# Performance work log

Hardware: AMD Instinct MI355X
Metric: run time of the kernel (lower is better)

## Reference

```python
import jax, jax.numpy as jnp
import numpy as np

D_MODEL = 1024
N_HEADS = 16
HEAD_DIM = D_MODEL // N_HEADS


def setup_inputs() -> dict:
    key = jax.random.key(0)
    ks = jax.random.split(key, 12)
    B, S = 2, 2048
    scale = 1.0 / np.sqrt(D_MODEL)
    inp = {
        "query": jax.random.normal(ks[0], (B, S, D_MODEL), jnp.float32),
        "key": jax.random.normal(ks[1], (B, S, D_MODEL), jnp.float32),
        "value": jax.random.normal(ks[2], (B, S, D_MODEL), jnp.float32),
        "Wq": jax.random.normal(ks[3], (D_MODEL, D_MODEL), jnp.float32) * scale,
        "bq": jnp.zeros((D_MODEL,), jnp.float32),
        "Wk": jax.random.normal(ks[4], (D_MODEL, D_MODEL), jnp.float32) * scale,
        "bk": jnp.zeros((D_MODEL,), jnp.float32),
        "Wv": jax.random.normal(ks[5], (D_MODEL, D_MODEL), jnp.float32) * scale,
        "bv": jnp.zeros((D_MODEL,), jnp.float32),
        "Wo": jax.random.normal(ks[6], (D_MODEL, D_MODEL), jnp.float32) * scale,
        "bo": jnp.zeros((D_MODEL,), jnp.float32),
    }
    return inp


def _split_heads(x):
    # [B, S, D] -> [B, H, S, Dh]
    B, S, _ = x.shape
    return x.reshape(B, S, N_HEADS, HEAD_DIM).transpose(0, 2, 1, 3)


def reference(query, key, value, Wq, bq, Wk, bk, Wv, bv, Wo, bo):
    B, S, _ = query.shape
    Q = _split_heads(query @ Wq + bq)   # [B,H,S,Dh]
    K = _split_heads(key @ Wk + bk)
    V = _split_heads(value @ Wv + bv)
    inv_sqrt_dh = 1.0 / np.sqrt(HEAD_DIM).astype(np.float32)
    scores = jnp.einsum("bhqd,bhkd->bhqk", Q, K) * inv_sqrt_dh
    attention = jax.nn.softmax(scores, axis=-1)
    # dropout is identity in eval mode
    out = jnp.einsum("bhqk,bhkd->bhqd", attention, V)
    out = out.transpose(0, 2, 1, 3).reshape(B, S, D_MODEL)
    out = out @ Wo + bo
    return out, attention
```

## Files before the change

kernel.cpp:

```cpp
#include <hip/hip_runtime.h>
#include <math.h>

#define D_MODEL 1024
#define NHEADS 16
#define HDIM 64
#define BATCH 2
#define SEQ 2048
#define MROWS (BATCH * SEQ)

typedef unsigned int uint32;
typedef __attribute__((ext_vector_type(8))) short short8;
typedef __attribute__((ext_vector_type(4))) float f32x4;
typedef __attribute__((ext_vector_type(16))) float f32x16;
typedef __attribute__((ext_vector_type(2))) unsigned int uint2v;

__device__ __forceinline__ unsigned short f2bf(float f) {
  unsigned int u = __float_as_uint(f);
  u += 0x7fffu + ((u >> 16) & 1u);
  return (unsigned short)(u >> 16);
}

__device__ __forceinline__ float fexp2(float x) {
  float r;
  asm("v_exp_f32 %0, %1" : "=v"(r) : "v"(x));
  return r;
}

__device__ __forceinline__ unsigned int cvtpk(float lo, float hi) {
  unsigned int r;
  asm("v_cvt_pk_bf16_f32 %0, %1, %2" : "=v"(r) : "v"(lo), "v"(hi));
  return r;
}

__device__ __forceinline__ void bar_lgkm() {
  asm volatile("s_waitcnt lgkmcnt(0)\n\ts_barrier" ::: "memory");
}

__device__ __forceinline__ void gl_lds16(const void* g, void* l) {
  __builtin_amdgcn_global_load_lds((const __attribute__((address_space(1))) void*)g,
                                   (__attribute__((address_space(3))) void*)l, 16, 0, 0);
}

__global__ __launch_bounds__(256) void conv_kernel(const float* q, const float* k, const float* v,
                                                   unsigned short* xq, unsigned short* xk,
                                                   unsigned short* xv) {
  int z = blockIdx.y;
  const float* s = (z == 0) ? q : ((z == 1) ? k : v);
  unsigned short* d = (z == 0) ? xq : ((z == 1) ? xk : xv);
  int i = (blockIdx.x * 256 + threadIdx.x) * 8;
  float4 v0 = *(const float4*)(s + i);
  float4 v1 = *(const float4*)(s + i + 4);
  uint4 o;
  o.x = cvtpk(v0.x, v0.y);
  o.y = cvtpk(v0.z, v0.w);
  o.z = cvtpk(v1.x, v1.y);
  o.w = cvtpk(v1.z, v1.w);
  *(uint4*)(d + i) = o;
}

struct WtArgs { const float* src[4]; };

__global__ __launch_bounds__(256) void wt_kernel(WtArgs args, unsigned short* dst) {
  const float* W = args.src[blockIdx.z];
  unsigned short* WT = dst + (size_t)blockIdx.z * (D_MODEL * D_MODEL);
  __shared__ unsigned short tile[64][80];
  int t = threadIdx.x;
  int r = t >> 2, cc = (t & 3) * 16;
  int k0 = blockIdx.y * 64, n0 = blockIdx.x * 64;
  const float* src = W + (size_t)(k0 + r) * D_MODEL + n0 + cc;
#pragma unroll
  for (int j = 0; j < 16; j += 4) {
    float4 v = *(const float4*)(src + j);
    tile[r][cc + j + 0] = f2bf(v.x);
    tile[r][cc + j + 1] = f2bf(v.y);
    tile[r][cc + j + 2] = f2bf(v.z);
    tile[r][cc + j + 3] = f2bf(v.w);
  }
  __syncthreads();
  __align__(16) unsigned short tmp[16];
#pragma unroll
  for (int j = 0; j < 16; ++j) tmp[j] = tile[cc + j][r];
  unsigned short* d = WT + (size_t)(n0 + r) * D_MODEL + k0 + cc;
  *(uint4*)d = ((uint4*)tmp)[0];
  *(uint4*)(d + 8) = ((uint4*)tmp)[1];
}

struct GemmArgs {
  const unsigned short* A[3];
  const unsigned short* W[3];
  const float* bias[3];
  void* C[3];
};

template <bool OUT_F32>
__global__ __launch_bounds__(256) void gemm_kernel(GemmArgs args) {
  int bid = blockIdx.x;
  int wgid = (bid & 7) * (gridDim.x >> 3) + (bid >> 3);
  int x = wgid & 7;
  int yz = wgid >> 3;
  int y = yz & 31;
  int z = yz >> 5;
  const unsigned short* A = args.A[z];
  const unsigned short* WT = args.W[z];
  const float* bias = args.bias[z];
  int n0 = x * 128, m0 = y * 128;
  __shared__ __align__(16) unsigned short As[128 * 64];
  __shared__ __align__(16) unsigned short Bs[128 * 64];
  int t = threadIdx.x;
  int wave = t >> 6, lane = t & 63;
  int wm = (wave >> 1) * 64, wn = (wave & 1) * 64;
  int lr = lane & 15, lg = lane >> 4;
  int r8 = lane >> 3, c8 = (lane & 7) * 8;
  f32x4 acc[4][4] = {};

  for (int kt = 0; kt < D_MODEL; kt += 64) {
#pragma unroll
    for (int i = 0; i < 4; ++i) {
      int row = wave * 32 + i * 8;
      gl_lds16(A + (size_t)(m0 + row + r8) * D_MODEL + kt + c8, As + row * 64);
      gl_lds16(WT + (size_t)(n0 + row + r8) * D_MODEL + kt + c8, Bs + row * 64);
    }
    __syncthreads();
    short8 af[4][2], bf[4][2];
#pragma unroll
    for (int f = 0; f < 4; ++f) {
#pragma unroll
      for (int kk = 0; kk < 2; ++kk) {
        af[f][kk] = *(const short8*)((const char*)As + (wm + f * 16 + lr) * 128 + kk * 64 + lg * 16);
        bf[f][kk] = *(const short8*)((const char*)Bs + (wn + f * 16 + lr) * 128 + kk * 64 + lg * 16);
      }
    }
#pragma unroll
    for (int i = 0; i < 4; ++i)
#pragma unroll
      for (int j = 0; j < 4; ++j)
#pragma unroll
        for (int kk = 0; kk < 2; ++kk)
          acc[i][j] = __builtin_amdgcn_mfma_f32_16x16x32_bf16(af[i][kk], bf[j][kk], acc[i][j], 0, 0, 0);
    __syncthreads();
  }
#pragma unroll
  for (int i = 0; i < 4; ++i)
#pragma unroll
    for (int j = 0; j < 4; ++j) {
      int col = n0 + wn + j * 16 + lr;
      float bb = bias[col];
#pragma unroll
      for (int r = 0; r < 4; ++r) {
        int row = m0 + wm + i * 16 + lg * 4 + r;
        float v = acc[i][j][r] + bb;
        if (OUT_F32)
          ((float*)args.C[z])[(size_t)row * D_MODEL + col] = v;
        else
          ((unsigned short*)args.C[z])[(size_t)row * D_MODEL + col] = f2bf(v);
      }
    }
}

__global__ __launch_bounds__(256) void vt_kernel(const unsigned short* V, unsigned short* Vt) {
  int bh = blockIdx.y;
  int b = bh >> 4;
  int h = bh & 15;
  int s0 = blockIdx.x * 64;
  __shared__ unsigned short tile[64][80];
  int t = threadIdx.x;
  int r = t >> 2, c = (t & 3) * 16;
  const unsigned short* src = V + (size_t)(b * SEQ + s0 + r) * D_MODEL + h * HDIM + c;
  __align__(16) unsigned short buf[16];
  ((uint4*)buf)[0] = *(const uint4*)src;
  ((uint4*)buf)[1] = *(const uint4*)(src + 8);
#pragma unroll
  for (int j = 0; j < 16; ++j) tile[r][c + j] = buf[j];
  __syncthreads();
  __align__(16) unsigned short tmp[16];
#pragma unroll
  for (int j = 0; j < 16; ++j) tmp[j] = tile[c + j][r];
  unsigned short* dst = Vt + ((size_t)bh * HDIM + r) * SEQ + s0 + c;
  *(uint4*)dst = ((uint4*)tmp)[0];
  *(uint4*)(dst + 8) = ((uint4*)tmp)[1];
}

__global__ __launch_bounds__(256) void attn_kernel(const unsigned short* Q, const unsigned short* K,
                                                   const unsigned short* Vt, float* attn,
                                                   unsigned short* ctx) {
  int bid = blockIdx.x;
  int wgid = (bid & 7) * 64 + (bid >> 3);
  int bh = wgid >> 4;
  int q0 = (wgid & 15) * 128;
  int b = bh >> 4, h = bh & 15;
  int t = threadIdx.x, wave = t >> 6, lane = t & 63;
  int l31 = lane & 31, hi = lane >> 5;

  __shared__ __align__(16) char Ks[2][64 * 128];
  __shared__ __align__(16) char Vs[2][64 * 128];

  const unsigned short* Kp = K + (size_t)(b * SEQ) * D_MODEL + h * HDIM;
  const unsigned short* Vp = Vt + (size_t)bh * HDIM * SEQ;

  short8 qv[4];
  {
    const unsigned short* qp = Q + (size_t)(b * SEQ + q0 + wave * 32 + l31) * D_MODEL + h * HDIM + hi * 8;
#pragma unroll
    for (int kk = 0; kk < 4; ++kk) qv[kk] = *(const short8*)(qp + kk * 16);
  }

  const float SCL = 0.125f * 1.44269504f;
  float lsum = 0.f;
  f32x16 oacc[2] = {};

#pragma unroll
  for (int c = 0; c < 2; ++c) {
    int idx = t + 256 * c;
    int row = idx >> 3, ch = idx & 7;
    int cb = (ch * 16) ^ ((row & 7) << 4);
    *(uint4*)(Ks[0] + row * 128 + cb) = *(const uint4*)(Kp + (size_t)row * D_MODEL + ch * 8);
    *(uint4*)(Vs[0] + row * 128 + cb) = *(const uint4*)(Vp + (size_t)row * SEQ + ch * 8);
  }
  bar_lgkm();
  int cur = 0;
  for (int ti = 0; ti < 32; ++ti) {
    uint4 nk[2], nv[2];
    bool more = (ti + 1) < 32;
    if (more) {
#pragma unroll
      for (int c = 0; c < 2; ++c) {
        int idx = t + 256 * c;
        int row = idx >> 3, ch = idx & 7;
        nk[c] = *(const uint4*)(Kp + (size_t)((ti + 1) * 64 + row) * D_MODEL + ch * 8);
        nv[c] = *(const uint4*)(Vp + (size_t)row * SEQ + (ti + 1) * 64 + ch * 8);
      }
    }
    f32x16 st[2] = {};
#pragma unroll
    for (int n = 0; n < 2; ++n)
#pragma unroll
      for (int kk = 0; kk < 4; ++kk) {
        int kr = n * 32 + l31;
        short8 ak = *(const short8*)(Ks[cur] + kr * 128 + ((kk * 32 + hi * 16) ^ ((kr & 7) << 4)));
        st[n] = __builtin_amdgcn_mfma_f32_32x32x16_bf16(ak, qv[kk], st[n], 0, 0, 0);
      }
    unsigned int P0[2][4], P1[2][4];
#pragma unroll
    for (int n = 0; n < 2; ++n)
#pragma unroll
      for (int j2 = 0; j2 < 4; ++j2) {
        float p0 = fexp2(st[n][4 * j2 + 0] * SCL);
        float p1 = fexp2(st[n][4 * j2 + 1] * SCL);
        float p2 = fexp2(st[n][4 * j2 + 2] * SCL);
        float p3 = fexp2(st[n][4 * j2 + 3] * SCL);
        lsum += (p0 + p1) + (p2 + p3);
        P0[n][j2] = cvtpk(p0, p1);
        P1[n][j2] = cvtpk(p2, p3);
      }
    short8 pa[4];
#pragma unroll
    for (int n = 0; n < 2; ++n)
#pragma unroll
      for (int c = 0; c < 2; ++c) {
        uint2v s0 = __builtin_amdgcn_permlane32_swap(P0[n][2 * c], P0[n][2 * c + 1], false, false);
        uint2v s1 = __builtin_amdgcn_permlane32_swap(P1[n][2 * c], P1[n][2 * c + 1], false, false);
        uint4 w;
        w.x = s0.x; w.y = s1.x; w.z = s0.y; w.w = s1.y;
        pa[n * 2 + c] = *(short8*)&w;
      }
#pragma unroll
    for (int n2 = 0; n2 < 2; ++n2)
#pragma unroll
      for (int kk = 0; kk < 4; ++kk) {
        int vr = n2 * 32 + l31;
        short8 bv = *(const short8*)(Vs[cur] + vr * 128 + ((kk * 32 + hi * 16) ^ ((vr & 7) << 4)));
        oacc[n2] = __builtin_amdgcn_mfma_f32_32x32x16_bf16(pa[kk], bv, oacc[n2], 0, 0, 0);
      }
    if (more) {
#pragma unroll
      for (int c = 0; c < 2; ++c) {
        int idx = t + 256 * c;
        int row = idx >> 3, ch = idx & 7;
        int cb = (ch * 16) ^ ((row & 7) << 4);
        *(uint4*)(Ks[cur ^ 1] + row * 128 + cb) = nk[c];
        *(uint4*)(Vs[cur ^ 1] + row * 128 + cb) = nv[c];
      }
    }
    bar_lgkm();
    cur ^= 1;
  }
  float tot = lsum + __shfl_xor(lsum, 32, 64);
  float inv = 1.f / tot;
  float iv16[16];
#pragma unroll
  for (int reg = 0; reg < 16; ++reg) {
    int qr = (reg & 3) + 8 * (reg >> 2) + 4 * hi;
    iv16[reg] = __shfl(inv, qr, 64);
  }
#pragma unroll
  for (int n2 = 0; n2 < 2; ++n2)
#pragma unroll
    for (int reg = 0; reg < 16; ++reg) {
      int qr = (reg & 3) + 8 * (reg >> 2) + 4 * hi;
      int row = b * SEQ + q0 + wave * 32 + qr;
      ctx[(size_t)row * D_MODEL + h * HDIM + n2 * 32 + l31] = f2bf(oacc[n2][reg] * iv16[reg]);
    }

  float* rowp[16];
  {
    float* abase = attn + (size_t)bh * SEQ * SEQ + l31;
#pragma unroll
    for (int reg = 0; reg < 16; ++reg) {
      int qr = (reg & 3) + 8 * (reg >> 2) + 4 * hi;
      rowp[reg] = abase + (size_t)(q0 + wave * 32 + qr) * SEQ;
    }
  }
#pragma unroll
  for (int c = 0; c < 2; ++c) {
    int idx = t + 256 * c;
    int row = idx >> 3, ch = idx & 7;
    int cb = (ch * 16) ^ ((row & 7) << 4);
    *(uint4*)(Ks[0] + row * 128 + cb) = *(const uint4*)(Kp + (size_t)row * D_MODEL + ch * 8);
  }
  bar_lgkm();
  cur = 0;
  for (int ti = 0; ti < 32; ++ti) {
    uint4 nk[2];
    bool more = (ti + 1) < 32;
    if (more) {
#pragma unroll
      for (int c = 0; c < 2; ++c) {
        int idx = t + 256 * c;
        int row = idx >> 3, ch = idx & 7;
        nk[c] = *(const uint4*)(Kp + (size_t)((ti + 1) * 64 + row) * D_MODEL + ch * 8);
      }
    }
    f32x16 st[2] = {};
#pragma unroll
    for (int n = 0; n < 2; ++n)
#pragma unroll
      for (int kk = 0; kk < 4; ++kk) {
        int kr = n * 32 + l31;
        short8 bk = *(const short8*)(Ks[cur] + kr * 128 + ((kk * 32 + hi * 16) ^ ((kr & 7) << 4)));
        st[n] = __builtin_amdgcn_mfma_f32_32x32x16_bf16(qv[kk], bk, st[n], 0, 0, 0);
      }
#pragma unroll
    for (int n = 0; n < 2; ++n)
#pragma unroll
      for (int reg = 0; reg < 16; ++reg) {
        float p = fexp2(st[n][reg] * SCL) * iv16[reg];
        __builtin_nontemporal_store(p, rowp[reg] + ti * 64 + n * 32);
      }
    if (more) {
#pragma unroll
      for (int c = 0; c < 2; ++c) {
        int idx = t + 256 * c;
        int row = idx >> 3, ch = idx & 7;
        int cb = (ch * 16) ^ ((row & 7) << 4);
        *(uint4*)(Ks[cur ^ 1] + row * 128 + cb) = nk[c];
      }
    }
    bar_lgkm();
    cur ^= 1;
  }
}

extern "C" void kernel_launch(void* const* d_in, const int* in_sizes, int n_in,
                              void* d_out, int out_size, void* d_ws, size_t ws_size,
                              hipStream_t stream) {
  const float* query = (const float*)d_in[0];
  const float* key   = (const float*)d_in[1];
  const float* value = (const float*)d_in[2];
  const float* Wq = (const float*)d_in[3];
  const float* bq = (const float*)d_in[4];
  const float* Wk = (const float*)d_in[5];
  const float* bk = (const float*)d_in[6];
  const float* Wv = (const float*)d_in[7];
  const float* bv = (const float*)d_in[8];
  const float* Wo = (const float*)d_in[9];
  const float* bo = (const float*)d_in[10];

  char* ws = (char*)d_ws;
  const size_t MB = (size_t)1 << 20;
  unsigned short* WqT = (unsigned short*)(ws + 0 * MB);
  unsigned short* WkT = (unsigned short*)(ws + 2 * MB);
  unsigned short* WvT = (unsigned short*)(ws + 4 * MB);
  unsigned short* WoT = (unsigned short*)(ws + 6 * MB);
  unsigned short* Xq  = (unsigned short*)(ws + 8 * MB);
  unsigned short* Xk  = (unsigned short*)(ws + 16 * MB);
  unsigned short* Xv  = (unsigned short*)(ws + 24 * MB);
  unsigned short* Qw  = (unsigned short*)(ws + 32 * MB);
  unsigned short* Kw  = (unsigned short*)(ws + 40 * MB);
  unsigned short* Vw  = (unsigned short*)(ws + 48 * MB);
  unsigned short* Vtw = (unsigned short*)(ws + 16 * MB);
  unsigned short* Cw  = (unsigned short*)(ws + 8 * MB);

  float* out0 = (float*)d_out;
  float* attn = out0 + (size_t)MROWS * D_MODEL;

  conv_kernel<<<dim3(2048, 3), 256, 0, stream>>>(query, key, value, Xq, Xk, Xv);

  WtArgs wa;
  wa.src[0] = Wq; wa.src[1] = Wk; wa.src[2] = Wv; wa.src[3] = Wo;
  wt_kernel<<<dim3(16, 16, 4), 256, 0, stream>>>(wa, WqT);

  GemmArgs ga;
  ga.A[0] = Xq; ga.A[1] = Xk; ga.A[2] = Xv;
  ga.W[0] = WqT; ga.W[1] = WkT; ga.W[2] = WvT;
  ga.bias[0] = bq; ga.bias[1] = bk; ga.bias[2] = bv;
  ga.C[0] = Qw; ga.C[1] = Kw; ga.C[2] = Vw;
  gemm_kernel<false><<<dim3(768), 256, 0, stream>>>(ga);

  vt_kernel<<<dim3(32, 32), 256, 0, stream>>>(Vw, Vtw);

  attn_kernel<<<dim3(512), 256, 0, stream>>>(Qw, Kw, Vtw, attn, Cw);

  GemmArgs go;
  go.A[0] = Cw; go.A[1] = Cw; go.A[2] = Cw;
  go.W[0] = WoT; go.W[1] = WoT; go.W[2] = WoT;
  go.bias[0] = bo; go.bias[1] = bo; go.bias[2] = bo;
  go.C[0] = d_out; go.C[1] = d_out; go.C[2] = d_out;
  gemm_kernel<true><<<dim3(256), 256, 0, stream>>>(go);
}
```

Baseline: 285.6 us.

## Split attention into context and weights kernels, read K/V directly from global

Result: slower. 354.4 us (+24.1%).

```diff
diff --git a/kernel.cpp b/kernel.cpp
--- a/kernel.cpp
+++ b/kernel.cpp
@@ -30,10 +30,6 @@
   unsigned int r;
   asm("v_cvt_pk_bf16_f32 %0, %1, %2" : "=v"(r) : "v"(lo), "v"(hi));
   return r;
-}
-
-__device__ __forceinline__ void bar_lgkm() {
-  asm volatile("s_waitcnt lgkmcnt(0)\n\ts_barrier" ::: "memory");
 }
 
 __device__ __forceinline__ void gl_lds16(const void* g, void* l) {
@@ -180,9 +176,9 @@
   *(uint4*)(dst + 8) = ((uint4*)tmp)[1];
 }
 
-__global__ __launch_bounds__(256) void attn_kernel(const unsigned short* Q, const unsigned short* K,
-                                                   const unsigned short* Vt, float* attn,
-                                                   unsigned short* ctx) {
+__global__ __launch_bounds__(256, 3) void attn_ctx_kernel(const unsigned short* Q, const unsigned short* K,
+                                                          const unsigned short* Vt, float* invl_g,
+                                                          unsigned short* ctx) {
   int bid = blockIdx.x;
   int wgid = (bid & 7) * 64 + (bid >> 3);
   int bh = wgid >> 4;
@@ -191,11 +187,8 @@
   int t = threadIdx.x, wave = t >> 6, lane = t & 63;
   int l31 = lane & 31, hi = lane >> 5;
 
-  __shared__ __align__(16) char Ks[2][64 * 128];
-  __shared__ __align__(16) char Vs[2][64 * 128];
-
-  const unsigned short* Kp = K + (size_t)(b * SEQ) * D_MODEL + h * HDIM;
-  const unsigned short* Vp = Vt + (size_t)bh * HDIM * SEQ;
+  const unsigned short* Kf = K + (size_t)(b * SEQ + l31) * D_MODEL + h * HDIM + hi * 8;
+  const unsigned short* Vf = Vt + ((size_t)bh * HDIM + l31) * SEQ + hi * 8;
 
   short8 qv[4];
   {
@@ -208,35 +201,13 @@
   float lsum = 0.f;
   f32x16 oacc[2] = {};
 
-#pragma unroll
-  for (int c = 0; c < 2; ++c) {
-    int idx = t + 256 * c;
-    int row = idx >> 3, ch = idx & 7;
-    int cb = (ch * 16) ^ ((row & 7) << 4);
-    *(uint4*)(Ks[0] + row * 128 + cb) = *(const uint4*)(Kp + (size_t)row * D_MODEL + ch * 8);
-    *(uint4*)(Vs[0] + row * 128 + cb) = *(const uint4*)(Vp + (size_t)row * SEQ + ch * 8);
-  }
-  bar_lgkm();
-  int cur = 0;
   for (int ti = 0; ti < 32; ++ti) {
-    uint4 nk[2], nv[2];
-    bool more = (ti + 1) < 32;
-    if (more) {
-#pragma unroll
-      for (int c = 0; c < 2; ++c) {
-        int idx = t + 256 * c;
-        int row = idx >> 3, ch = idx & 7;
-        nk[c] = *(const uint4*)(Kp + (size_t)((ti + 1) * 64 + row) * D_MODEL + ch * 8);
-        nv[c] = *(const uint4*)(Vp + (size_t)row * SEQ + (ti + 1) * 64 + ch * 8);
-      }
-    }
     f32x16 st[2] = {};
 #pragma unroll
     for (int n = 0; n < 2; ++n)
 #pragma unroll
       for (int kk = 0; kk < 4; ++kk) {
-        int kr = n * 32 + l31;
-        short8 ak = *(const short8*)(Ks[cur] + kr * 128 + ((kk * 32 + hi * 16) ^ ((kr & 7) << 4)));
+        short8 ak = *(const short8*)(Kf + (size_t)(ti * 64 + n * 32) * D_MODEL + kk * 16);
         st[n] = __builtin_amdgcn_mfma_f32_32x32x16_bf16(ak, qv[kk], st[n], 0, 0, 0);
       }
     unsigned int P0[2][4], P1[2][4];
@@ -267,25 +238,13 @@
     for (int n2 = 0; n2 < 2; ++n2)
 #pragma unroll
       for (int kk = 0; kk < 4; ++kk) {
-        int vr = n2 * 32 + l31;
-        short8 bv = *(const short8*)(Vs[cur] + vr * 128 + ((kk * 32 + hi * 16) ^ ((vr & 7) << 4)));
+        short8 bv = *(const short8*)(Vf + (size_t)(n2 * 32) * SEQ + ti * 64 + kk * 16);
         oacc[n2] = __builtin_amdgcn_mfma_f32_32x32x16_bf16(pa[kk], bv, oacc[n2], 0, 0, 0);
       }
-    if (more) {
-#pragma unroll
-      for (int c = 0; c < 2; ++c) {
-        int idx = t + 256 * c;
-        int row = idx >> 3, ch = idx & 7;
-        int cb = (ch * 16) ^ ((row & 7) << 4);
-        *(uint4*)(Ks[cur ^ 1] + row * 128 + cb) = nk[c];
-        *(uint4*)(Vs[cur ^ 1] + row * 128 + cb) = nv[c];
-      }
-    }
-    bar_lgkm();
-    cur ^= 1;
   }
   float tot = lsum + __shfl_xor(lsum, 32, 64);
   float inv = 1.f / tot;
+  if (lane < 32) invl_g[(size_t)bh * SEQ + q0 + wave * 32 + l31] = inv;
   float iv16[16];
 #pragma unroll
   for (int reg = 0; reg < 16; ++reg) {
@@ -300,63 +259,51 @@
       int row = b * SEQ + q0 + wave * 32 + qr;
       ctx[(size_t)row * D_MODEL + h * HDIM + n2 * 32 + l31] = f2bf(oacc[n2][reg] * iv16[reg]);
     }
-
-  float* rowp[16];
+}
+
+__global__ __launch_bounds__(256, 4) void attn_w_kernel(const unsigned short* Q, const unsigned short* K,
+                                                        const float* invl_g, float* attn) {
+  int bid = blockIdx.x;
+  int wgid = (bid & 7) * 64 + (bid >> 3);
+  int bh = wgid >> 4;
+  int q0 = (wgid & 15) * 128;
+  int b = bh >> 4, h = bh & 15;
+  int t = threadIdx.x, wave = t >> 6, lane = t & 63;
+  int l31 = lane & 31, hi = lane >> 5;
+
+  const unsigned short* Kf = K + (size_t)(b * SEQ + l31) * D_MODEL + h * HDIM + hi * 8;
+
+  short8 qv[4];
   {
-    float* abase = attn + (size_t)bh * SEQ * SEQ + l31;
-#pragma unroll
-    for (int reg = 0; reg < 16; ++reg) {
-      int qr = (reg & 3) + 8 * (reg >> 2) + 4 * hi;
-      rowp[reg] = abase + (size_t)(q0 + wave * 32 + qr) * SEQ;
-    }
-  }
-#pragma unroll
-  for (int c = 0; c < 2; ++c) {
-    int idx = t + 256 * c;
-    int row = idx >> 3, ch = idx & 7;
-    int cb = (ch * 16) ^ ((row & 7) << 4);
-    *(uint4*)(Ks[0] + row * 128 + cb) = *(const uint4*)(Kp + (size_t)row * D_MODEL + ch * 8);
-  }
-  bar_lgkm();
-  cur = 0;
+    const unsigned short* qp = Q + (size_t)(b * SEQ + q0 + wave * 32 + l31) * D_MODEL + h * HDIM + hi * 8;
+#pragma unroll
+    for (int kk = 0; kk < 4; ++kk) qv[kk] = *(const short8*)(qp + kk * 16);
+  }
+  float4 invl4[4];
+#pragma unroll
+  for (int j2 = 0; j2 < 4; ++j2)
+    invl4[j2] = *(const float4*)(invl_g + (size_t)bh * SEQ + q0 + wave * 32 + 8 * j2 + 4 * hi);
+
+  float* abase = attn + (size_t)bh * SEQ * SEQ + (size_t)(q0 + wave * 32 + 4 * hi) * SEQ + l31;
+  const float SCL = 0.125f * 1.44269504f;
+
   for (int ti = 0; ti < 32; ++ti) {
-    uint4 nk[2];
-    bool more = (ti + 1) < 32;
-    if (more) {
-#pragma unroll
-      for (int c = 0; c < 2; ++c) {
-        int idx = t + 256 * c;
-        int row = idx >> 3, ch = idx & 7;
-        nk[c] = *(const uint4*)(Kp + (size_t)((ti + 1) * 64 + row) * D_MODEL + ch * 8);
-      }
-    }
     f32x16 st[2] = {};
 #pragma unroll
     for (int n = 0; n < 2; ++n)
 #pragma unroll
       for (int kk = 0; kk < 4; ++kk) {
-        int kr = n * 32 + l31;
-        short8 bk = *(const short8*)(Ks[cur] + kr * 128 + ((kk * 32 + hi * 16) ^ ((kr & 7) << 4)));
+        short8 bk = *(const short8*)(Kf + (size_t)(ti * 64 + n * 32) * D_MODEL + kk * 16);
         st[n] = __builtin_amdgcn_mfma_f32_32x32x16_bf16(qv[kk], bk, st[n], 0, 0, 0);
       }
+    float* tb = abase + ti * 64;
 #pragma unroll
     for (int n = 0; n < 2; ++n)
 #pragma unroll
       for (int reg = 0; reg < 16; ++reg) {
-        float p = fexp2(st[n][reg] * SCL) * iv16[reg];
-        __builtin_nontemporal_store(p, rowp[reg] + ti * 64 + n * 32);
-      }
-    if (more) {
-#pragma unroll
-      for (int c = 0; c < 2; ++c) {
-        int idx = t + 256 * c;
-        int row = idx >> 3, ch = idx & 7;
-        int cb = (ch * 16) ^ ((row & 7) << 4);
-        *(uint4*)(Ks[cur ^ 1] + row * 128 + cb) = nk[c];
-      }
-    }
-    bar_lgkm();
-    cur ^= 1;
+        float p = fexp2(st[n][reg] * SCL) * invl4[reg >> 2][reg & 3];
+        __builtin_nontemporal_store(p, tb + ((reg & 3) + 8 * (reg >> 2)) * SEQ + n * 32);
+      }
   }
 }
 
@@ -389,6 +336,7 @@
   unsigned short* Vw  = (unsigned short*)(ws + 48 * MB);
   unsigned short* Vtw = (unsigned short*)(ws + 16 * MB);
   unsigned short* Cw  = (unsigned short*)(ws + 8 * MB);
+  float* invl_g       = (float*)(ws + 56 * MB);
 
   float* out0 = (float*)d_out;
   float* attn = out0 + (size_t)MROWS * D_MODEL;
@@ -408,7 +356,8 @@
 
   vt_kernel<<<dim3(32, 32), 256, 0, stream>>>(Vw, Vtw);
 
-  attn_kernel<<<dim3(512), 256, 0, stream>>>(Qw, Kw, Vtw, attn, Cw);
+  attn_ctx_kernel<<<dim3(512), 256, 0, stream>>>(Qw, Kw, Vtw, invl_g, Cw);
+  attn_w_kernel<<<dim3(512), 256, 0, stream>>>(Qw, Kw, invl_g, attn);
 
   GemmArgs go;
   go.A[0] = Cw; go.A[1] = Cw; go.A[2] = Cw;
```

## Fuse prep kernels and compute V transposed directly in QKV GEMM

Applied to the files above, without the earlier changes.

After: 280.2 us. No clear change (-1.9%).

```diff
diff --git a/kernel.cpp b/kernel.cpp
--- a/kernel.cpp
+++ b/kernel.cpp
@@ -41,48 +41,54 @@
                                    (__attribute__((address_space(3))) void*)l, 16, 0, 0);
 }
 
-__global__ __launch_bounds__(256) void conv_kernel(const float* q, const float* k, const float* v,
-                                                   unsigned short* xq, unsigned short* xk,
-                                                   unsigned short* xv) {
-  int z = blockIdx.y;
-  const float* s = (z == 0) ? q : ((z == 1) ? k : v);
-  unsigned short* d = (z == 0) ? xq : ((z == 1) ? xk : xv);
-  int i = (blockIdx.x * 256 + threadIdx.x) * 8;
-  float4 v0 = *(const float4*)(s + i);
-  float4 v1 = *(const float4*)(s + i + 4);
-  uint4 o;
-  o.x = cvtpk(v0.x, v0.y);
-  o.y = cvtpk(v0.z, v0.w);
-  o.z = cvtpk(v1.x, v1.y);
-  o.w = cvtpk(v1.z, v1.w);
-  *(uint4*)(d + i) = o;
-}
-
-struct WtArgs { const float* src[4]; };
-
-__global__ __launch_bounds__(256) void wt_kernel(WtArgs args, unsigned short* dst) {
-  const float* W = args.src[blockIdx.z];
-  unsigned short* WT = dst + (size_t)blockIdx.z * (D_MODEL * D_MODEL);
-  __shared__ unsigned short tile[64][80];
+struct PrepArgs {
+  const float* act[3];
+  unsigned short* actout[3];
+  const float* w[4];
+  unsigned short* wout;
+};
+
+__global__ __launch_bounds__(256) void prep_kernel(PrepArgs args) {
+  int bid = blockIdx.x;
   int t = threadIdx.x;
-  int r = t >> 2, cc = (t & 3) * 16;
-  int k0 = blockIdx.y * 64, n0 = blockIdx.x * 64;
-  const float* src = W + (size_t)(k0 + r) * D_MODEL + n0 + cc;
-#pragma unroll
-  for (int j = 0; j < 16; j += 4) {
-    float4 v = *(const float4*)(src + j);
-    tile[r][cc + j + 0] = f2bf(v.x);
-    tile[r][cc + j + 1] = f2bf(v.y);
-    tile[r][cc + j + 2] = f2bf(v.z);
-    tile[r][cc + j + 3] = f2bf(v.w);
-  }
-  __syncthreads();
-  __align__(16) unsigned short tmp[16];
-#pragma unroll
-  for (int j = 0; j < 16; ++j) tmp[j] = tile[cc + j][r];
-  unsigned short* d = WT + (size_t)(n0 + r) * D_MODEL + k0 + cc;
-  *(uint4*)d = ((uint4*)tmp)[0];
-  *(uint4*)(d + 8) = ((uint4*)tmp)[1];
+  if (bid < 6144) {
+    int z = bid >> 11, blk = bid & 2047;
+    const float* s = args.act[z];
+    unsigned short* d = args.actout[z];
+    int i = (blk * 256 + t) * 8;
+    float4 v0 = *(const float4*)(s + i);
+    float4 v1 = *(const float4*)(s + i + 4);
+    uint4 o;
+    o.x = cvtpk(v0.x, v0.y);
+    o.y = cvtpk(v0.z, v0.w);
+    o.z = cvtpk(v1.x, v1.y);
+    o.w = cvtpk(v1.z, v1.w);
+    *(uint4*)(d + i) = o;
+  } else {
+    __shared__ unsigned short tile[64][80];
+    int wb = bid - 6144;
+    int zz = wb >> 8, rem = wb & 255;
+    int n0 = (rem & 15) * 64, k0 = (rem >> 4) * 64;
+    const float* W = args.w[zz];
+    unsigned short* WT = args.wout + (size_t)zz * (D_MODEL * D_MODEL);
+    int r = t >> 2, cc = (t & 3) * 16;
+    const float* src = W + (size_t)(k0 + r) * D_MODEL + n0 + cc;
+#pragma unroll
+    for (int j = 0; j < 16; j += 4) {
+      float4 v = *(const float4*)(src + j);
+      tile[r][cc + j + 0] = f2bf(v.x);
+      tile[r][cc + j + 1] = f2bf(v.y);
+      tile[r][cc + j + 2] = f2bf(v.z);
+      tile[r][cc + j + 3] = f2bf(v.w);
+    }
+    __syncthreads();
+    __align__(16) unsigned short tmp[16];
+#pragma unroll
+    for (int j = 0; j < 16; ++j) tmp[j] = tile[cc + j][r];
+    unsigned short* d = WT + (size_t)(n0 + r) * D_MODEL + k0 + cc;
+    *(uint4*)d = ((uint4*)tmp)[0];
+    *(uint4*)(d + 8) = ((uint4*)tmp)[1];
+  }
 }
 
 struct GemmArgs {
@@ -92,17 +98,273 @@
   void* C[3];
 };
 
-template <bool OUT_F32>
-__global__ __launch_bounds__(256) void gemm_kernel(GemmArgs args) {
+__global__ __launch_bounds__(256) void gemm_qkv_kernel(GemmArgs args) {
   int bid = blockIdx.x;
-  int wgid = (bid & 7) * (gridDim.x >> 3) + (bid >> 3);
-  int x = wgid & 7;
-  int yz = wgid >> 3;
-  int y = yz & 31;
-  int z = yz >> 5;
-  const unsigned short* A = args.A[z];
-  const unsigned short* WT = args.W[z];
-  const float* bias = args.bias[z];
+  int wgid = (bid & 7) * 96 + (bid >> 3);
+  const unsigned short *A, *WT;
+  const float* bias;
+  void* C;
+  int m0, n0;
+  bool vtrans;
+  if (wgid < 512) {
+    int x = wgid & 7, yz = wgid >> 3, y = yz & 31, z = yz >> 5;
+    A = args.A[z]; WT = args.W[z]; bias = args.bias[z]; C = args.C[z];
+    n0 = x * 128; m0 = y * 128; vtrans = false;
+  } else {
+    int w2 = wgid - 512, x2 = w2 & 31, y2 = w2 >> 5;
+    A = args.W[2];
+    WT = args.A[2];
+    bias = args.bias[2]; C = args.C[2];
+    n0 = x2 * 128; m0 = y2 * 128; vtrans = true;
+  }
+  __shared__ __align__(16) unsigned short As[128 * 64];
+  __shared__ __align__(16) unsigned short Bs[128 * 64];
+  int t = threadIdx.x;
+  int wave = t >> 6, lane = t & 63;
+  int wm = (wave >> 1) * 64, wn = (wave & 1) * 64;
+  int lr = lane & 15, lg = lane >> 4;
+  int r8 = lane >> 3, c8 = (lane & 7) * 8;
+  f32x4 acc[4][4] = {};
+
+  for (int kt = 0; kt < D_MODEL; kt += 64) {
+#pragma unroll
+    for (int i = 0; i < 4; ++i) {
+      int row = wave * 32 + i * 8;
+      gl_lds16(A + (size_t)(m0 + row + r8) * D_MODEL + kt + c8, As + row * 64);
+      gl_lds16(WT + (size_t)(n0 + row + r8) * D_MODEL + kt + c8, Bs + row * 64);
+    }
+    __syncthreads();
+    short8 af[4][2], bf[4][2];
+#pragma unroll
+    for (int f = 0; f < 4; ++f) {
+#pragma unroll
+      for (int kk = 0; kk < 2; ++kk) {
+        af[f][kk] = *(const short8*)((const char*)As + (wm + f * 16 + lr) * 128 + kk * 64 + lg * 16);
+        bf[f][kk] = *(const short8*)((const char*)Bs + (wn + f * 16 + lr) * 128 + kk * 64 + lg * 16);
+      }
+    }
+#pragma unroll
+    for (int i = 0; i < 4; ++i)
+#pragma unroll
+      for (int j = 0; j < 4; ++j)
+#pragma unroll
+        for (int kk = 0; kk < 2; ++kk)
+          acc[i][j] = __builtin_amdgcn_mfma_f32_16x16x32_bf16(af[i][kk], bf[j][kk], acc[i][j], 0, 0, 0);
+    __syncthreads();
+  }
+  if (!vtrans) {
+#pragma unroll
+    for (int i = 0; i < 4; ++i)
+#pragma unroll
+      for (int j = 0; j < 4; ++j) {
+        int col = n0 + wn + j * 16 + lr;
+        float bb = bias[col];
+#pragma unroll
+        for (int r = 0; r < 4; ++r) {
+          int row = m0 + wm + i * 16 + lg * 4 + r;
+          ((unsigned short*)C)[(size_t)row * D_MODEL + col] = f2bf(acc[i][j][r] + bb);
+        }
+      }
+  } else {
+#pragma unroll
+    for (int i = 0; i < 4; ++i)
+#pragma unroll
+      for (int j = 0; j < 4; ++j) {
+        int col = n0 + wn + j * 16 + lr;
+#pragma unroll
+        for (int r = 0; r < 4; ++r) {
+          int row = m0 + wm + i * 16 + lg * 4 + r;
+          ((unsigned short*)C)[(size_t)row * MROWS + col] = f2bf(acc[i][j][r] + bias[row]);
+        }
+      }
+  }
+}
+
+__global__ __launch_bounds__(256) void attn_kernel(const unsigned short* Q, const unsigned short* K,
+                                                   const unsigned short* Vt2, float* attn,
+                                                   unsigned short* ctx) {
+  int bid = blockIdx.x;
+  int wgid = (bid & 7) * 64 + (bid >> 3);
+  int bh = wgid >> 4;
+  int q0 = (wgid & 15) * 128;
+  int b = bh >> 4, h = bh & 15;
+  int t = threadIdx.x, wave = t >> 6, lane = t & 63;
+  int l31 = lane & 31, hi = lane >> 5;
+
+  __shared__ __align__(16) char Ks[2][64 * 128];
+  __shared__ __align__(16) char Vs[2][64 * 128];
+
+  const unsigned short* Kp = K + (size_t)(b * SEQ) * D_MODEL + h * HDIM;
+  const unsigned short* Vp = Vt2 + (size_t)(h * HDIM) * MROWS + b * SEQ;
+
+  short8 qv[4];
+  {
+    const unsigned short* qp = Q + (size_t)(b * SEQ + q0 + wave * 32 + l31) * D_MODEL + h * HDIM + hi * 8;
+#pragma unroll
+    for (int kk = 0; kk < 4; ++kk) qv[kk] = *(const short8*)(qp + kk * 16);
+  }
+
+  const float SCL = 0.125f * 1.44269504f;
+  float lsum = 0.f;
+  f32x16 oacc[2] = {};
+
+#pragma unroll
+  for (int c = 0; c < 2; ++c) {
+    int idx = t + 256 * c;
+    int row = idx >> 3, ch = idx & 7;
+    int cb = (ch * 16) ^ ((row & 7) << 4);
+    *(uint4*)(Ks[0] + row * 128 + cb) = *(const uint4*)(Kp + (size_t)row * D_MODEL + ch * 8);
+    *(uint4*)(Vs[0] + row * 128 + cb) = *(const uint4*)(Vp + (size_t)row * MROWS + ch * 8);
+  }
+  bar_lgkm();
+  int cur = 0;
+  for (int ti = 0; ti < 32; ++ti) {
+    uint4 nk[2], nv[2];
+    bool more = (ti + 1) < 32;
+    if (more) {
+#pragma unroll
+      for (int c = 0; c < 2; ++c) {
+        int idx = t + 256 * c;
+        int row = idx >> 3, ch = idx & 7;
+        nk[c] = *(const uint4*)(Kp + (size_t)((ti + 1) * 64 + row) * D_MODEL + ch * 8);
+        nv[c] = *(const uint4*)(Vp + (size_t)row * MROWS + (ti + 1) * 64 + ch * 8);
+      }
+    }
+    f32x16 st[2] = {};
+#pragma unroll
+    for (int n = 0; n < 2; ++n)
+#pragma unroll
+      for (int kk = 0; kk < 4; ++kk) {
+        int kr = n * 32 + l31;
+        short8 ak = *(const short8*)(Ks[cur] + kr * 128 + ((kk * 32 + hi * 16) ^ ((kr & 7) << 4)));
+        st[n] = __builtin_amdgcn_mfma_f32_32x32x16_bf16(ak, qv[kk], st[n], 0, 0, 0);
+      }
+    unsigned int P0[2][4], P1[2][4];
+#pragma unroll
+    for (int n = 0; n < 2; ++n)
+#pragma unroll
+      for (int j2 = 0; j2 < 4; ++j2) {
+        float p0 = fexp2(st[n][4 * j2 + 0] * SCL);
+        float p1 = fexp2(st[n][4 * j2 + 1] * SCL);
+        float p2 = fexp2(st[n][4 * j2 + 2] * SCL);
+        float p3 = fexp2(st[n][4 * j2 + 3] * SCL);
+        lsum += (p0 + p1) + (p2 + p3);
+        P0[n][j2] = cvtpk(p0, p1);
+        P1[n][j2] = cvtpk(p2, p3);
+      }
+    short8 pa[4];
+#pragma unroll
+    for (int n = 0; n < 2; ++n)
+#pragma unroll
+      for (int c = 0; c < 2; ++c) {
+        uint2v s0 = __builtin_amdgcn_permlane32_swap(P0[n][2 * c], P0[n][2 * c + 1], false, false);
+        uint2v s1 = __builtin_amdgcn_permlane32_swap(P1[n][2 * c], P1[n][2 * c + 1], false, false);
+        uint4 w;
+        w.x = s0.x; w.y = s1.x; w.z = s0.y; w.w = s1.y;
+        pa[n * 2 + c] = *(short8*)&w;
+      }
+#pragma unroll
+    for (int n2 = 0; n2 < 2; ++n2)
+#pragma unroll
+      for (int kk = 0; kk < 4; ++kk) {
+        int vr = n2 * 32 + l31;
+        short8 bv = *(const short8*)(Vs[cur] + vr * 128 + ((kk * 32 + hi * 16) ^ ((vr & 7) << 4)));
+        oacc[n2] = __builtin_amdgcn_mfma_f32_32x32x16_bf16(pa[kk], bv, oacc[n2], 0, 0, 0);
+      }
+    if (more) {
+#pragma unroll
+      for (int c = 0; c < 2; ++c) {
+        int idx = t + 256 * c;
+        int row = idx >> 3, ch = idx & 7;
+        int cb = (ch * 16) ^ ((row & 7) << 4);
+        *(uint4*)(Ks[cur ^ 1] + row * 128 + cb) = nk[c];
+        *(uint4*)(Vs[cur ^ 1] + row * 128 + cb) = nv[c];
+      }
+    }
+    bar_lgkm();
+    cur ^= 1;
+  }
+  float tot = lsum + __shfl_xor(lsum, 32, 64);
+  float inv = 1.f / tot;
+  float iv16[16];
+#pragma unroll
+  for (int reg = 0; reg < 16; ++reg) {
+    int qr = (reg & 3) + 8 * (reg >> 2) + 4 * hi;
+    iv16[reg] = __shfl(inv, qr, 64);
+  }
+#pragma unroll
+  for (int n2 = 0; n2 < 2; ++n2)
+#pragma unroll
+    for (int reg = 0; reg < 16; ++reg) {
+      int qr = (reg & 3) + 8 * (reg >> 2) + 4 * hi;
+      int row = b * SEQ + q0 + wave * 32 + qr;
+      ctx[(size_t)row * D_MODEL + h * HDIM + n2 * 32 + l31] = f2bf(oacc[n2][reg] * iv16[reg]);
+    }
+
+  float* rowp[16];
+  {
+    float* abase = attn + (size_t)bh * SEQ * SEQ + l31;
+#pragma unroll
+    for (int reg = 0; reg < 16; ++reg) {
+      int qr = (reg & 3) + 8 * (reg >> 2) + 4 * hi;
+      rowp[reg] = abase + (size_t)(q0 + wave * 32 + qr) * SEQ;
+    }
+  }
+#pragma unroll
+  for (int c = 0; c < 2; ++c) {
+    int idx = t + 256 * c;
+    int row = idx >> 3, ch = idx & 7;
+    int cb = (ch * 16) ^ ((row & 7) << 4);
+    *(uint4*)(Ks[0] + row * 128 + cb) = *(const uint4*)(Kp + (size_t)row * D_MODEL + ch * 8);
+  }
+  bar_lgkm();
+  cur = 0;
+  for (int ti = 0; ti < 32; ++ti) {
+    uint4 nk[2];
+    bool more = (ti + 1) < 32;
+    if (more) {
+#pragma unroll
+      for (int c = 0; c < 2; ++c) {
+        int idx = t + 256 * c;
+        int row = idx >> 3, ch = idx & 7;
+        nk[c] = *(const uint4*)(Kp + (size_t)((ti + 1) * 64 + row) * D_MODEL + ch * 8);
+      }
+    }
+    f32x16 st[2] = {};
+#pragma unroll
+    for (int n = 0; n < 2; ++n)
+#pragma unroll
+      for (int kk = 0; kk < 4; ++kk) {
+        int kr = n * 32 + l31;
+        short8 bk = *(const short8*)(Ks[cur] + kr * 128 + ((kk * 32 + hi * 16) ^ ((kr & 7) << 4)));
+        st[n] = __builtin_amdgcn_mfma_f32_32x32x16_bf16(qv[kk], bk, st[n], 0, 0, 0);
+      }
+#pragma unroll
+    for (int n = 0; n < 2; ++n)
+#pragma unroll
+      for (int reg = 0; reg < 16; ++reg) {
+        float p = fexp2(st[n][reg] * SCL) * iv16[reg];
+        __builtin_nontemporal_store(p, rowp[reg] + ti * 64 + n * 32);
+      }
+    if (more) {
+#pragma unroll
+      for (int c = 0; c < 2; ++c) {
+        int idx = t + 256 * c;
+        int row = idx >> 3, ch = idx & 7;
+        int cb = (ch * 16) ^ ((row & 7) << 4);
+        *(uint4*)(Ks[cur ^ 1] + row * 128 + cb) = nk[c];
+      }
+    }
+    bar_lgkm();
+    cur ^= 1;
+  }
+}
+
+__global__ __launch_bounds__(256) void gemm_o_kernel(const unsigned short* A, const unsigned short* WT,
+                                                     const float* bias, float* C) {
+  int bid = blockIdx.x;
+  int wgid = (bid & 7) * 32 + (bid >> 3);
+  int x = wgid & 7, y = wgid >> 3;
   int n0 = x * 128, m0 = y * 128;
   __shared__ __align__(16) unsigned short As[128 * 64];
   __shared__ __align__(16) unsigned short Bs[128 * 64];
@@ -148,216 +410,9 @@
 #pragma unroll
       for (int r = 0; r < 4; ++r) {
         int row = m0 + wm + i * 16 + lg * 4 + r;
-        float v = acc[i][j][r] + bb;
-        if (OUT_F32)
-          ((float*)args.C[z])[(size_t)row * D_MODEL + col] = v;
-        else
-          ((unsigned short*)args.C[z])[(size_t)row * D_MODEL + col] = f2bf(v);
-      }
-    }
-}
-
-__global__ __launch_bounds__(256) void vt_kernel(const unsigned short* V, unsigned short* Vt) {
-  int bh = blockIdx.y;
-  int b = bh >> 4;
-  int h = bh & 15;
-  int s0 = blockIdx.x * 64;
-  __shared__ unsigned short tile[64][80];
-  int t = threadIdx.x;
-  int r = t >> 2, c = (t & 3) * 16;
-  const unsigned short* src = V + (size_t)(b * SEQ + s0 + r) * D_MODEL + h * HDIM + c;
-  __align__(16) unsigned short buf[16];
-  ((uint4*)buf)[0] = *(const uint4*)src;
-  ((uint4*)buf)[1] = *(const uint4*)(src + 8);
-#pragma unroll
-  for (int j = 0; j < 16; ++j) tile[r][c + j] = buf[j];
-  __syncthreads();
-  __align__(16) unsigned short tmp[16];
-#pragma unroll
-  for (int j = 0; j < 16; ++j) tmp[j] = tile[c + j][r];
-  unsigned short* dst = Vt + ((size_t)bh * HDIM + r) * SEQ + s0 + c;
-  *(uint4*)dst = ((uint4*)tmp)[0];
-  *(uint4*)(dst + 8) = ((uint4*)tmp)[1];
-}
-
-__global__ __launch_bounds__(256) void attn_kernel(const unsigned short* Q, const unsigned short* K,
-                                                   const unsigned short* Vt, float* attn,
-                                                   unsigned short* ctx) {
-  int bid = blockIdx.x;
-  int wgid = (bid & 7) * 64 + (bid >> 3);
-  int bh = wgid >> 4;
-  int q0 = (wgid & 15) * 128;
-  int b = bh >> 4, h = bh & 15;
-  int t = threadIdx.x, wave = t >> 6, lane = t & 63;
-  int l31 = lane & 31, hi = lane >> 5;
-
-  __shared__ __align__(16) char Ks[2][64 * 128];
-  __shared__ __align__(16) char Vs[2][64 * 128];
-
-  const unsigned short* Kp = K + (size_t)(b * SEQ) * D_MODEL + h * HDIM;
-  const unsigned short* Vp = Vt + (size_t)bh * HDIM * SEQ;
-
-  short8 qv[4];
-  {
-    const unsigned short* qp = Q + (size_t)(b * SEQ + q0 + wave * 32 + l31) * D_MODEL + h * HDIM + hi * 8;
-#pragma unroll
-    for (int kk = 0; kk < 4; ++kk) qv[kk] = *(const short8*)(qp + kk * 16);
-  }
-
-  const float SCL = 0.125f * 1.44269504f;
-  float lsum = 0.f;
-  f32x16 oacc[2] = {};
-
-#pragma unroll
-  for (int c = 0; c < 2; ++c) {
-    int idx = t + 256 * c;
-    int row = idx >> 3, ch = idx & 7;
-    int cb = (ch * 16) ^ ((row & 7) << 4);
-    *(uint4*)(Ks[0] + row * 128 + cb) = *(const uint4*)(Kp + (size_t)row * D_MODEL + ch * 8);
-    *(uint4*)(Vs[0] + row * 128 + cb) = *(const uint4*)(Vp + (size_t)row * SEQ + ch * 8);
-  }
-  bar_lgkm();
-  int cur = 0;
-  for (int ti = 0; ti < 32; ++ti) {
-    uint4 nk[2], nv[2];
-    bool more = (ti + 1) < 32;
-    if (more) {
-#pragma unroll
-      for (int c = 0; c < 2; ++c) {
-        int idx = t + 256 * c;
-        int row = idx >> 3, ch = idx & 7;
-        nk[c] = *(const uint4*)(Kp + (size_t)((ti + 1) * 64 + row) * D_MODEL + ch * 8);
-        nv[c] = *(const uint4*)(Vp + (size_t)row * SEQ + (ti + 1) * 64 + ch * 8);
-      }
-    }
-    f32x16 st[2] = {};
-#pragma unroll
-    for (int n = 0; n < 2; ++n)
-#pragma unroll
-      for (int kk = 0; kk < 4; ++kk) {
-        int kr = n * 32 + l31;
-        short8 ak = *(const short8*)(Ks[cur] + kr * 128 + ((kk * 32 + hi * 16) ^ ((kr & 7) << 4)));
-        st[n] = __builtin_amdgcn_mfma_f32_32x32x16_bf16(ak, qv[kk], st[n], 0, 0, 0);
-      }
-    unsigned int P0[2][4], P1[2][4];
-#pragma unroll
-    for (int n = 0; n < 2; ++n)
-#pragma unroll
-      for (int j2 = 0; j2 < 4; ++j2) {
-        float p0 = fexp2(st[n][4 * j2 + 0] * SCL);
-        float p1 = fexp2(st[n][4 * j2 + 1] * SCL);
-        float p2 = fexp2(st[n][4 * j2 + 2] * SCL);
-        float p3 = fexp2(st[n][4 * j2 + 3] * SCL);
-        lsum += (p0 + p1) + (p2 + p3);
-        P0[n][j2] = cvtpk(p0, p1);
-        P1[n][j2] = cvtpk(p2, p3);
-      }
-    short8 pa[4];
-#pragma unroll
-    for (int n = 0; n < 2; ++n)
-#pragma unroll
-      for (int c = 0; c < 2; ++c) {
-        uint2v s0 = __builtin_amdgcn_permlane32_swap(P0[n][2 * c], P0[n][2 * c + 1], false, false);
-        uint2v s1 = __builtin_amdgcn_permlane32_swap(P1[n][2 * c], P1[n][2 * c + 1], false, false);
-        uint4 w;
-        w.x = s0.x; w.y = s1.x; w.z = s0.y; w.w = s1.y;
-        pa[n * 2 + c] = *(short8*)&w;
-      }
-#pragma unroll
-    for (int n2 = 0; n2 < 2; ++n2)
-#pragma unroll
-      for (int kk = 0; kk < 4; ++kk) {
-        int vr = n2 * 32 + l31;
-        short8 bv = *(const short8*)(Vs[cur] + vr * 128 + ((kk * 32 + hi * 16) ^ ((vr & 7) << 4)));
-        oacc[n2] = __builtin_amdgcn_mfma_f32_32x32x16_bf16(pa[kk], bv, oacc[n2], 0, 0, 0);
-      }
-    if (more) {
-#pragma unroll
-      for (int c = 0; c < 2; ++c) {
-        int idx = t + 256 * c;
-        int row = idx >> 3, ch = idx & 7;
-        int cb = (ch * 16) ^ ((row & 7) << 4);
-        *(uint4*)(Ks[cur ^ 1] + row * 128 + cb) = nk[c];
-        *(uint4*)(Vs[cur ^ 1] + row * 128 + cb) = nv[c];
-      }
-    }
-    bar_lgkm();
-    cur ^= 1;
-  }
-  float tot = lsum + __shfl_xor(lsum, 32, 64);
-  float inv = 1.f / tot;
-  float iv16[16];
-#pragma unroll
-  for (int reg = 0; reg < 16; ++reg) {
-    int qr = (reg & 3) + 8 * (reg >> 2) + 4 * hi;
-    iv16[reg] = __shfl(inv, qr, 64);
-  }
-#pragma unroll
-  for (int n2 = 0; n2 < 2; ++n2)
-#pragma unroll
-    for (int reg = 0; reg < 16; ++reg) {
-      int qr = (reg & 3) + 8 * (reg >> 2) + 4 * hi;
-      int row = b * SEQ + q0 + wave * 32 + qr;
-      ctx[(size_t)row * D_MODEL + h * HDIM + n2 * 32 + l31] = f2bf(oacc[n2][reg] * iv16[reg]);
-    }
-
-  float* rowp[16];
-  {
-    float* abase = attn + (size_t)bh * SEQ * SEQ + l31;
-#pragma unroll
-    for (int reg = 0; reg < 16; ++reg) {
-      int qr = (reg & 3) + 8 * (reg >> 2) + 4 * hi;
-      rowp[reg] = abase + (size_t)(q0 + wave * 32 + qr) * SEQ;
-    }
-  }
-#pragma unroll
-  for (int c = 0; c < 2; ++c) {
-    int idx = t + 256 * c;
-    int row = idx >> 3, ch = idx & 7;
-    int cb = (ch * 16) ^ ((row & 7) << 4);
-    *(uint4*)(Ks[0] + row * 128 + cb) = *(const uint4*)(Kp + (size_t)row * D_MODEL + ch * 8);
-  }
-  bar_lgkm();
-  cur = 0;
-  for (int ti = 0; ti < 32; ++ti) {
-    uint4 nk[2];
-    bool more = (ti + 1) < 32;
-    if (more) {
-#pragma unroll
-      for (int c = 0; c < 2; ++c) {
-        int idx = t + 256 * c;
-        int row = idx >> 3, ch = idx & 7;
-        nk[c] = *(const uint4*)(Kp + (size_t)((ti + 1) * 64 + row) * D_MODEL + ch * 8);
-      }
-    }
-    f32x16 st[2] = {};
-#pragma unroll
-    for (int n = 0; n < 2; ++n)
-#pragma unroll
-      for (int kk = 0; kk < 4; ++kk) {
-        int kr = n * 32 + l31;
-        short8 bk = *(const short8*)(Ks[cur] + kr * 128 + ((kk * 32 + hi * 16) ^ ((kr & 7) << 4)));
-        st[n] = __builtin_amdgcn_mfma_f32_32x32x16_bf16(qv[kk], bk, st[n], 0, 0, 0);
-      }
-#pragma unroll
-    for (int n = 0; n < 2; ++n)
-#pragma unroll
-      for (int reg = 0; reg < 16; ++reg) {
-        float p = fexp2(st[n][reg] * SCL) * iv16[reg];
-        __builtin_nontemporal_store(p, rowp[reg] + ti * 64 + n * 32);
-      }
-    if (more) {
-#pragma unroll
-      for (int c = 0; c < 2; ++c) {
-        int idx = t + 256 * c;
-        int row = idx >> 3, ch = idx & 7;
-        int cb = (ch * 16) ^ ((row & 7) << 4);
-        *(uint4*)(Ks[cur ^ 1] + row * 128 + cb) = nk[c];
-      }
-    }
-    bar_lgkm();
-    cur ^= 1;
-  }
+        C[(size_t)row * D_MODEL + col] = acc[i][j][r] + bb;
+      }
+    }
 }
 
 extern "C" void kernel_launch(void* const* d_in, const int* in_sizes, int n_in,
@@ -378,7 +433,6 @@
   char* ws = (char*)d_ws;
   const size_t MB = (size_t)1 << 20;
   unsigned short* WqT = (unsigned short*)(ws + 0 * MB);
-  unsigned short* WkT = (unsigned short*)(ws + 2 * MB);
   unsigned short* WvT = (unsigned short*)(ws + 4 * MB);
   unsigned short* WoT = (unsigned short*)(ws + 6 * MB);
   unsigned short* Xq  = (unsigned short*)(ws + 8 * MB);
@@ -386,34 +440,27 @@
   unsigned short* Xv  = (unsigned short*)(ws + 24 * MB);
   unsigned short* Qw  = (unsigned short*)(ws + 32 * MB);
   unsigned short* Kw  = (unsigned short*)(ws + 40 * MB);
-  unsigned short* Vw  = (unsigned short*)(ws + 48 * MB);
-  unsigned short* Vtw = (unsigned short*)(ws + 16 * MB);
+  unsigned short* Vt2 = (unsigned short*)(ws + 48 * MB);
   unsigned short* Cw  = (unsigned short*)(ws + 8 * MB);
 
   float* out0 = (float*)d_out;
   float* attn = out0 + (size_t)MROWS * D_MODEL;
 
-  conv_kernel<<<dim3(2048, 3), 256, 0, stream>>>(query, key, value, Xq, Xk, Xv);
-
-  WtArgs wa;
-  wa.src[0] = Wq; wa.src[1] = Wk; wa.src[2] = Wv; wa.src[3] = Wo;
-  wt_kernel<<<dim3(16, 16, 4), 256, 0, stream>>>(wa, WqT);
+  PrepArgs pa;
+  pa.act[0] = query; pa.act[1] = key; pa.act[2] = value;
+  pa.actout[0] = Xq; pa.actout[1] = Xk; pa.actout[2] = Xv;
+  pa.w[0] = Wq; pa.w[1] = Wk; pa.w[2] = Wv; pa.w[3] = Wo;
+  pa.wout = WqT;
+  prep_kernel<<<dim3(7168), 256, 0, stream>>>(pa);
 
   GemmArgs ga;
   ga.A[0] = Xq; ga.A[1] = Xk; ga.A[2] = Xv;
-  ga.W[0] = WqT; ga.W[1] = WkT; ga.W[2] = WvT;
+  ga.W[0] = WqT; ga.W[1] = WqT + (size_t)D_MODEL * D_MODEL; ga.W[2] = WvT;
   ga.bias[0] = bq; ga.bias[1] = bk; ga.bias[2] = bv;
-  ga.C[0] = Qw; ga.C[1] = Kw; ga.C[2] = Vw;
-  gemm_kernel<false><<<dim3(768), 256, 0, stream>>>(ga);
-
-  vt_kernel<<<dim3(32, 32), 256, 0, stream>>>(Vw, Vtw);
-
-  attn_kernel<<<dim3(512), 256, 0, stream>>>(Qw, Kw, Vtw, attn, Cw);
-
-  GemmArgs go;
-  go.A[0] = Cw; go.A[1] = Cw; go.A[2] = Cw;
-  go.W[0] = WoT; go.W[1] = WoT; go.W[2] = WoT;
-  go.bias[0] = bo; go.bias[1] = bo; go.bias[2] = bo;
-  go.C[0] = d_out; go.C[1] = d_out; go.C[2] = d_out;
-  gemm_kernel<true><<<dim3(256), 256, 0, stream>>>(go);
-}
+  ga.C[0] = Qw; ga.C[1] = Kw; ga.C[2] = Vt2;
+  gemm_qkv_kernel<<<dim3(768), 256, 0, stream>>>(ga);
+
+  attn_kernel<<<dim3(512), 256, 0, stream>>>(Qw, Kw, Vt2, attn, Cw);
+
+  gemm_o_kernel<<<dim3(256), 256, 0, stream>>>(Cw, WoT, bo, out0);
+}
```
